# Kernel optimization log

Measured on AMD Instinct MI355X. Metric: run time of the kernel, lower is better.

## Reference

```python
import jax, jax.numpy as jnp
import numpy as np
import math

NUM_HEADS = 8


def setup_inputs() -> dict:
    key = jax.random.key(0)
    ks = jax.random.split(key, 6)
    b, s, e = 4, 2048, 512
    x = jax.random.normal(ks[0], (b, s, e), dtype=jnp.float32)
    # 0/1 adjacency matrix as float (it multiplies the scores in the module)
    adj = jax.random.randint(ks[1], (b, s, s), 0, 2).astype(jnp.float32)
    scale = 0.02
    Wqkv_w = jax.random.normal(ks[2], (3 * e, e), dtype=jnp.float32) * scale
    Wqkv_b = jax.random.normal(ks[3], (3 * e,), dtype=jnp.float32) * scale
    out_w = jax.random.normal(ks[4], (e, e), dtype=jnp.float32) * scale
    out_b = jax.random.normal(ks[5], (e,), dtype=jnp.float32) * scale
    return {"x": x, "adj": adj, "Wqkv_w": Wqkv_w, "Wqkv_b": Wqkv_b,
            "out_w": out_w, "out_b": out_b}


def reference(x, adj, Wqkv_w, Wqkv_b, out_w, out_b):
    b, s, e = x.shape
    h = NUM_HEADS
    d = e // h
    # fused qkv projection: (b, s, 3*e) -> (b, s, 3, h, d)
    qkv = (x @ Wqkv_w.T + Wqkv_b).reshape(b, s, 3, h, d)
    qkv = jnp.transpose(qkv, (2, 0, 3, 1, 4))  # (3, b, h, s, d)
    q, k, v = qkv[0], qkv[1], qkv[2]
    inv_sqrt_d = 1.0 / math.sqrt(d)
    scores = jnp.einsum('bhqd,bhkd->bhqk', q, k) * inv_sqrt_d
    scores = jnp.clip(scores * adj[:, None, :, :], -10000.0, 10000.0)
    attn = jax.nn.softmax(scores, axis=-1)
    out = jnp.einsum('bhqk,bhkd->bhqd', attn, v)
    out = jnp.transpose(out, (0, 2, 1, 3)).reshape(b, s, e)  # (b, s, h*d)
    return out @ out_w.T + out_b
```

## Files before the change

### kernel.cpp

```cpp
#include <hip/hip_runtime.h>


typedef __attribute__((ext_vector_type(8))) short bf16x8;
typedef __attribute__((ext_vector_type(4))) float f32x4;
typedef __attribute__((ext_vector_type(4))) unsigned short ushort4v;
typedef __attribute__((ext_vector_type(4))) _Float16 f16x4;
typedef __attribute__((ext_vector_type(8))) _Float16 f16x8;
typedef __attribute__((ext_vector_type(2))) __fp16 h16x2;

#if __has_builtin(__builtin_amdgcn_exp2f)
#define EXP2F(x) __builtin_amdgcn_exp2f(x)
#else
#define EXP2F(x) exp2f(x)
#endif

#define QSCALE 0.18033688011112042f

__device__ __forceinline__ unsigned short f2bf(float f) {
  unsigned int u = __float_as_uint(f);
  u += 0x7FFFu + ((u >> 16) & 1u);
  return (unsigned short)(u >> 16);
}
__device__ __forceinline__ unsigned short f2h(float f) {
  union { _Float16 h; unsigned short u; } cv;
  cv.h = (_Float16)f;
  return cv.u;
}

__device__ __forceinline__ int sbit(unsigned w, int pos) {
  return ((int)(w << (31 - pos))) >> 31;
}

__device__ __forceinline__ f16x8 pk8(const float* p) {
  union { struct { h16x2 a, b, c, d; } s; f16x8 v; } u;
  u.s.a = __builtin_amdgcn_cvt_pkrtz(p[0], p[1]);
  u.s.b = __builtin_amdgcn_cvt_pkrtz(p[2], p[3]);
  u.s.c = __builtin_amdgcn_cvt_pkrtz(p[4], p[5]);
  u.s.d = __builtin_amdgcn_cvt_pkrtz(p[6], p[7]);
  return u.v;
}

__device__ __forceinline__ f32x4 mfma_pv(f16x8 a, f16x8 b, f32x4 c) {
#if __has_builtin(__builtin_amdgcn_mfma_f32_16x16x32_f16)
  return __builtin_amdgcn_mfma_f32_16x16x32_f16(a, b, c, 0, 0, 0);
#else
  union { f16x8 v; struct { f16x4 lo, hi; } s; } ua, ub;
  ua.v = a; ub.v = b;
  c = __builtin_amdgcn_mfma_f32_16x16x16f16(ua.s.lo, ub.s.lo, c, 0, 0, 0);
  return __builtin_amdgcn_mfma_f32_16x16x16f16(ua.s.hi, ub.s.hi, c, 0, 0, 0);
#endif
}

__global__ __launch_bounds__(256) void prep_k(const float* __restrict__ x,
                                              unsigned short* __restrict__ x_bf,
                                              const float* __restrict__ wqkv,
                                              unsigned short* __restrict__ wqkv_bf,
                                              const float* __restrict__ outw,
                                              unsigned short* __restrict__ outw_bf,
                                              const float* __restrict__ adj,
                                              unsigned long long* __restrict__ abits) {
  const int bid = blockIdx.x;
  if (bid < 5120) {
    const float* in; unsigned short* out; int i;
    if (bid < 4096) { in = x; out = x_bf; i = bid * 256 + threadIdx.x; }
    else if (bid < 4864) { in = wqkv; out = wqkv_bf; i = (bid - 4096) * 256 + threadIdx.x; }
    else { in = outw; out = outw_bf; i = (bid - 4864) * 256 + threadIdx.x; }
    float4 v = ((const float4*)in)[i];
    ushort4v o;
    o[0] = f2bf(v.x); o[1] = f2bf(v.y); o[2] = f2bf(v.z); o[3] = f2bf(v.w);
    ((ushort4v*)out)[i] = o;
  } else {
    const int gw = (bid - 5120) * 4 + (threadIdx.x >> 6);
    const int l = threadIdx.x & 63;
    const int b = gw >> 11, q = gw & 2047;
    const float* row = adj + ((size_t)b * 2048 + q) * 2048;
    unsigned long long* ob = abits + (size_t)b * 65536 + q;
#pragma unroll 4
    for (int kt = 0; kt < 32; ++kt) {
      const float v = row[kt * 64 + l];
      const unsigned long long m = __ballot(v != 0.f);
      if (l == 0) ob[(size_t)kt * 2048] = m;
    }
  }
}

template <int MODE>
__global__ __launch_bounds__(256, 3) void gemm128_k(const unsigned short* __restrict__ A,
                                                    const unsigned short* __restrict__ Bt,
                                                    const float* __restrict__ bias, int Kdim,
                                                    int Ntiles, unsigned short* __restrict__ q_out,
                                                    unsigned short* __restrict__ k_out,
                                                    unsigned short* __restrict__ v_out,
                                                    float* __restrict__ f_out) {
  __shared__ union {
    struct { unsigned short A[2][128][40], B[2][128][40]; } s;
    unsigned short T[64][136];
  } u;

  const int t = threadIdx.x;
  const int lane = t & 63, w = t >> 6, ln = lane & 15, quad = lane >> 4;
  const int xcd = blockIdx.x & 7, loc = blockIdx.x >> 3;
  const int mt = xcd * ((gridDim.x >> 3) / Ntiles) + loc / Ntiles;
  const int nt = loc % Ntiles;
  const int wm = (w >> 1) * 64, wn = (w & 1) * 64;
  const int strow = t >> 2, stcol = (t & 3) * 8;

  const size_t abase = (size_t)(mt * 128 + strow) * Kdim + stcol;
  const size_t bbase = (size_t)(nt * 128 + strow) * Kdim + stcol;

  f32x4 acc[4][4];
#pragma unroll
  for (int i = 0; i < 4; ++i)
#pragma unroll
    for (int j = 0; j < 4; ++j) acc[i][j] = (f32x4){0.f, 0.f, 0.f, 0.f};

  bf16x8 a0 = *(const bf16x8*)(A + abase);
  bf16x8 a1 = *(const bf16x8*)(A + abase + (size_t)64 * Kdim);
  bf16x8 b0 = *(const bf16x8*)(Bt + bbase);
  bf16x8 b1 = *(const bf16x8*)(Bt + bbase + (size_t)64 * Kdim);
  *(bf16x8*)&u.s.A[0][strow][stcol] = a0;
  *(bf16x8*)&u.s.A[0][64 + strow][stcol] = a1;
  *(bf16x8*)&u.s.B[0][strow][stcol] = b0;
  *(bf16x8*)&u.s.B[0][64 + strow][stcol] = b1;
  __syncthreads();

  const int iters = Kdim >> 5;
  for (int it = 0; it < iters; ++it) {
    const int cur = it & 1, nxt = cur ^ 1;

    const int kn = ((it + 1) << 5) & (Kdim - 1);
    a0 = *(const bf16x8*)(A + abase + kn);
    a1 = *(const bf16x8*)(A + abase + (size_t)64 * Kdim + kn);
    b0 = *(const bf16x8*)(Bt + bbase + kn);
    b1 = *(const bf16x8*)(Bt + bbase + (size_t)64 * Kdim + kn);

    bf16x8 bfr[4];
#pragma unroll
    for (int nf = 0; nf < 4; ++nf)
      bfr[nf] = *(const bf16x8*)&u.s.B[cur][wn + nf * 16 + ln][quad * 8];
#pragma unroll
    for (int mf = 0; mf < 4; ++mf) {
      bf16x8 af = *(const bf16x8*)&u.s.A[cur][wm + mf * 16 + ln][quad * 8];
#pragma unroll
      for (int nf = 0; nf < 4; ++nf)
        acc[mf][nf] = __builtin_amdgcn_mfma_f32_16x16x32_bf16(af, bfr[nf], acc[mf][nf], 0, 0, 0);
    }

    if (it + 1 < iters) {
      *(bf16x8*)&u.s.A[nxt][strow][stcol] = a0;
      *(bf16x8*)&u.s.A[nxt][64 + strow][stcol] = a1;
      *(bf16x8*)&u.s.B[nxt][strow][stcol] = b0;
      *(bf16x8*)&u.s.B[nxt][64 + strow][stcol] = b1;
      __syncthreads();
    }
  }

  if (MODE == 0 && nt >= 8) {
    const int bb = mt >> 4, sq0 = (mt & 15) * 128;
#pragma unroll
    for (int half = 0; half < 2; ++half) {
      __syncthreads();
      if ((w & 1) == half) {
#pragma unroll
        for (int nf = 0; nf < 4; ++nf) {
          const float bv = bias[nt * 128 + half * 64 + nf * 16 + ln];
#pragma unroll
          for (int mf = 0; mf < 4; ++mf)
#pragma unroll
            for (int r = 0; r < 4; ++r)
              u.T[nf * 16 + ln][wm + mf * 16 + quad * 4 + r] = f2h(acc[mf][nf][r] + bv);
        }
      }
      __syncthreads();
#pragma unroll
      for (int rep = 0; rep < 4; ++rep) {
        const int row = rep * 16 + (t >> 4), c = t & 15;
        const bf16x8 val = *(const bf16x8*)&u.T[row][c * 8];
        const int hd = (nt - 8) * 128 + half * 64 + row;
        const int hh = hd >> 6, dd = hd & 63;
        *(bf16x8*)(v_out + ((size_t)(bb * 8 + hh) * 64 + dd) * 2048 + sq0 + c * 8) = val;
      }
    }
    return;
  }

#pragma unroll
  for (int mf = 0; mf < 4; ++mf) {
    const int m = mt * 128 + wm + mf * 16 + quad * 4;
#pragma unroll
    for (int nf = 0; nf < 4; ++nf) {
      const int n = nt * 128 + wn + nf * 16 + ln;
      const float bv = bias[n];
      if (MODE == 0) {
        const int hd = n & 511;
        const int hh = hd >> 6, dd = hd & 63;
        const int bb = m >> 11, sq = m & 2047;
        if (n < 512) {
#pragma unroll
          for (int r = 0; r < 4; ++r)
            q_out[((size_t)(bb * 8 + hh) * 2048 + sq + r) * 64 + dd] =
                f2bf((acc[mf][nf][r] + bv) * QSCALE);
        } else {
#pragma unroll
          for (int r = 0; r < 4; ++r)
            k_out[((size_t)(bb * 8 + hh) * 2048 + sq + r) * 64 + dd] = f2bf(acc[mf][nf][r] + bv);
        }
      } else {
#pragma unroll
        for (int r = 0; r < 4; ++r) f_out[(size_t)(m + r) * 512 + n] = acc[mf][nf][r] + bv;
      }
    }
  }
}

__global__ __launch_bounds__(256, 2) void attn_k(const unsigned short* __restrict__ Qg,
                                                 const unsigned short* __restrict__ Kg,
                                                 const unsigned short* __restrict__ Vg,
                                                 const unsigned long long* __restrict__ Mg,
                                                 unsigned short* __restrict__ Og) {
  __shared__ unsigned short K_lds[2][64][64];
  __shared__ unsigned short V_lds[2][64][64];

  const int t = threadIdx.x;
  const int w = t >> 6, lane = t & 63, ln = lane & 15, quad = lane >> 4;
  const int bh = blockIdx.x & 31, qt = blockIdx.x >> 5, bb = bh >> 3;
  const int sbase = qt * 128;

  const unsigned short* Qp = Qg + (size_t)bh * (2048 * 64);
  const unsigned short* Kp = Kg + (size_t)bh * (2048 * 64);
  const unsigned short* Vp = Vg + (size_t)bh * (64 * 2048);
  const unsigned long long* Mw = Mg + (size_t)bb * 65536 + sbase + w * 32 + ln;

  bf16x8 qf[2][2];
#pragma unroll
  for (int qg = 0; qg < 2; ++qg) {
    const int qrow = sbase + w * 32 + qg * 16 + ln;
    qf[qg][0] = *(const bf16x8*)(Qp + (size_t)qrow * 64 + quad * 8);
    qf[qg][1] = *(const bf16x8*)(Qp + (size_t)qrow * 64 + 32 + quad * 8);
  }

  const _Float16 one_h = (_Float16)((ln == 0) ? 1.0f : 0.0f);
  const f16x8 vf_one = (f16x8){one_h, one_h, one_h, one_h, one_h, one_h, one_h, one_h};

  const f32x4 zf = (f32x4){0.f, 0.f, 0.f, 0.f};

  f32x4 acc_o[2][4];
#pragma unroll
  for (int qg = 0; qg < 2; ++qg)
#pragma unroll
    for (int dg = 0; dg < 4; ++dg) acc_o[qg][dg] = zf;
  f32x4 acc_1[2] = {zf, zf};

  const int strow = t >> 2;
  const int stcol = (t & 3) * 16;
  const int c0 = (t & 3) * 2;
  const int gkw = (strow & 3) | (((strow >> 3) & 1) << 2);
  const int gvw = strow & 7;

  const unsigned short* Kl = Kp + (size_t)strow * 64 + stcol;
  const unsigned short* Vl = Vp + (size_t)strow * 2048 + stcol;

  bf16x8 kr0 = *(const bf16x8*)(Kl);
  bf16x8 kr1 = *(const bf16x8*)(Kl + 8);
  bf16x8 vr0 = *(const bf16x8*)(Vl);
  bf16x8 vr1 = *(const bf16x8*)(Vl + 8);
  *(bf16x8*)&K_lds[0][strow][(c0 ^ gkw) << 3] = kr0;
  *(bf16x8*)&K_lds[0][strow][((c0 + 1) ^ gkw) << 3] = kr1;
  *(bf16x8*)&V_lds[0][strow][(c0 ^ gvw) << 3] = vr0;
  *(bf16x8*)&V_lds[0][strow][((c0 + 1) ^ gvw) << 3] = vr1;
  unsigned long long m0 = Mw[0], m1 = Mw[16];
  __syncthreads();

  const int kperm = ((ln >> 2) << 3) + (ln & 3);
  const int gkr = (ln & 3) | (((ln >> 2) & 1) << 2);
  const int gvr = ln & 7;
  const int kc = (quad ^ gkr) << 3;

#pragma unroll 2
  for (int kt = 0; kt < 32; ++kt) {
    const int cur = kt & 1, nxt = cur ^ 1;

    kr0 = *(const bf16x8*)(Kl + (size_t)(kt + 1) * 4096);
    kr1 = *(const bf16x8*)(Kl + (size_t)(kt + 1) * 4096 + 8);
    vr0 = *(const bf16x8*)(Vl + (kt + 1) * 64);
    vr1 = *(const bf16x8*)(Vl + (kt + 1) * 64 + 8);
    const unsigned long long m0n = Mw[(size_t)(kt + 1) * 2048];
    const unsigned long long m1n = Mw[(size_t)(kt + 1) * 2048 + 16];

    f32x4 sc[2][4];
    __builtin_amdgcn_s_setprio(1);
#pragma unroll
    for (int h = 0; h < 2; ++h)
#pragma unroll
      for (int e = 0; e < 2; ++e) {
        const int krow = h * 32 + kperm + e * 4;
        bf16x8 kf0 = *(const bf16x8*)&K_lds[cur][krow][kc];
        bf16x8 kf1 = *(const bf16x8*)&K_lds[cur][krow][kc ^ 32];
#pragma unroll
        for (int qg = 0; qg < 2; ++qg) {
          f32x4 z = __builtin_amdgcn_mfma_f32_16x16x32_bf16(kf0, qf[qg][0], zf, 0, 0, 0);
          sc[qg][h * 2 + e] = __builtin_amdgcn_mfma_f32_16x16x32_bf16(kf1, qf[qg][1], z, 0, 0, 0);
        }
      }
    __builtin_amdgcn_s_setprio(0);

    f16x8 vfa[2][4];
#pragma unroll
    for (int h = 0; h < 2; ++h)
#pragma unroll
      for (int dg = 0; dg < 4; ++dg)
        vfa[h][dg] = *(const f16x8*)&V_lds[cur][dg * 16 + ln][((h * 4 + quad) ^ gvr) << 3];

    f16x8 pa[2][2];
#pragma unroll
    for (int qg = 0; qg < 2; ++qg) {
      const unsigned long long m64 = qg ? m1 : m0;
#pragma unroll
      for (int h = 0; h < 2; ++h) {
        const unsigned wrd = (h ? (unsigned)(m64 >> 32) : (unsigned)m64) >> (quad * 8);
        float p[8];
#pragma unroll
        for (int e = 0; e < 2; ++e)
#pragma unroll
          for (int r = 0; r < 4; ++r) {
            const int j = e * 4 + r;
            const int se = sbit(wrd, j);
            const float s = __int_as_float(__float_as_int(sc[qg][h * 2 + e][r]) & se);
            p[j] = EXP2F(s);
          }
        pa[qg][h] = pk8(p);
      }
    }

    __builtin_amdgcn_s_setprio(1);
#pragma unroll
    for (int h = 0; h < 2; ++h)
#pragma unroll
      for (int qg = 0; qg < 2; ++qg) {
#pragma unroll
        for (int dg = 0; dg < 4; ++dg)
          acc_o[qg][dg] = mfma_pv(pa[qg][h], vfa[h][dg], acc_o[qg][dg]);
        acc_1[qg] = mfma_pv(pa[qg][h], vf_one, acc_1[qg]);
      }
    __builtin_amdgcn_s_setprio(0);

    if (kt < 31) {
      *(bf16x8*)&K_lds[nxt][strow][(c0 ^ gkw) << 3] = kr0;
      *(bf16x8*)&K_lds[nxt][strow][((c0 + 1) ^ gkw) << 3] = kr1;
      *(bf16x8*)&V_lds[nxt][strow][(c0 ^ gvw) << 3] = vr0;
      *(bf16x8*)&V_lds[nxt][strow][((c0 + 1) ^ gvw) << 3] = vr1;
      __syncthreads();
    }
    m0 = m0n;
    m1 = m1n;
  }

  unsigned short* Op = Og + (size_t)bb * 2048 * 512 + (size_t)(bh & 7) * 64;
#pragma unroll
  for (int qg = 0; qg < 2; ++qg)
#pragma unroll
    for (int r = 0; r < 4; ++r) {
      const float inv = 1.0f / __shfl(acc_1[qg][r], quad * 16);
      const int sq = sbase + w * 32 + qg * 16 + quad * 4 + r;
#pragma unroll
      for (int dg = 0; dg < 4; ++dg)
        Op[(size_t)sq * 512 + dg * 16 + ln] = f2bf(acc_o[qg][dg][r] * inv);
    }
}

extern "C" void kernel_launch(void* const* d_in, const int* in_sizes, int n_in, void* d_out,
                              int out_size, void* d_ws, size_t ws_size, hipStream_t stream) {
  const float* x = (const float*)d_in[0];
  const float* adj = (const float*)d_in[1];
  const float* wqkv = (const float*)d_in[2];
  const float* bqkv = (const float*)d_in[3];
  const float* outw = (const float*)d_in[4];
  const float* outb = (const float*)d_in[5];
  float* out = (float*)d_out;

  char* ws = (char*)d_ws;
  unsigned short* x_bf = (unsigned short*)(ws);
  unsigned short* wqkv_bf = (unsigned short*)(ws + 8388608);
  unsigned short* outw_bf = (unsigned short*)(ws + 9961472);
  unsigned long long* abits = (unsigned long long*)(ws + 10485760);
  unsigned short* Qb = (unsigned short*)(ws + 27262976);
  unsigned short* Kb = (unsigned short*)(ws + 35651584);
  unsigned short* Vb = (unsigned short*)(ws + 44040192);
  unsigned short* Ob = (unsigned short*)(ws + 52428800);

  prep_k<<<7168, 256, 0, stream>>>(x, x_bf, wqkv, wqkv_bf, outw, outw_bf, adj, abits);

  gemm128_k<0><<<768, 256, 0, stream>>>(x_bf, wqkv_bf, bqkv, 512, 12, Qb, Kb, Vb, nullptr);

  attn_k<<<512, 256, 0, stream>>>(Qb, Kb, Vb, abits, Ob);

  gemm128_k<1><<<256, 256, 0, stream>>>(Ob, outw_bf, outb, 512, 4, nullptr, nullptr, nullptr, out);
}
```

Before: 210.7 us.

## Fuse fp32-to-bf16 conversion and adjacency bitpacking into the QKV GEMM launch

Removes the separate prep kernel. The GEMMs now load fp32 x and weights directly and convert them to bf16 in registers with v_cvt_pk_bf16_f32. The adjacency ballot bitpacking runs in extra blocks appended to the QKV GEMM grid. This saves one launch and the bf16 round-trip through memory, but each GEMM block re-reads fp32 operands at twice the bytes and converts them redundantly. The bitpack blocks also share the grid with the GEMM tiles. Tile mapping and K are now hardcoded to 512.

```diff
diff --git a/kernel.cpp b/kernel.cpp
--- a/kernel.cpp
+++ b/kernel.cpp
@@ -25,6 +25,20 @@
   union { _Float16 h; unsigned short u; } cv;
   cv.h = (_Float16)f;
   return cv.u;
+}
+
+__device__ __forceinline__ unsigned cvtpk_bf16(float a, float b) {
+  unsigned r;
+  asm("v_cvt_pk_bf16_f32 %0, %1, %2" : "=v"(r) : "v"(a), "v"(b));
+  return r;
+}
+__device__ __forceinline__ bf16x8 cvt8(float4 lo, float4 hi) {
+  union { unsigned u[4]; bf16x8 v; } r;
+  r.u[0] = cvtpk_bf16(lo.x, lo.y);
+  r.u[1] = cvtpk_bf16(lo.z, lo.w);
+  r.u[2] = cvtpk_bf16(hi.x, hi.y);
+  r.u[3] = cvtpk_bf16(hi.z, hi.w);
+  return r.v;
 }
 
 __device__ __forceinline__ int sbit(unsigned w, int pos) {
@@ -51,62 +65,52 @@
 #endif
 }
 
-__global__ __launch_bounds__(256) void prep_k(const float* __restrict__ x,
-                                              unsigned short* __restrict__ x_bf,
-                                              const float* __restrict__ wqkv,
-                                              unsigned short* __restrict__ wqkv_bf,
-                                              const float* __restrict__ outw,
-                                              unsigned short* __restrict__ outw_bf,
-                                              const float* __restrict__ adj,
-                                              unsigned long long* __restrict__ abits) {
-  const int bid = blockIdx.x;
-  if (bid < 5120) {
-    const float* in; unsigned short* out; int i;
-    if (bid < 4096) { in = x; out = x_bf; i = bid * 256 + threadIdx.x; }
-    else if (bid < 4864) { in = wqkv; out = wqkv_bf; i = (bid - 4096) * 256 + threadIdx.x; }
-    else { in = outw; out = outw_bf; i = (bid - 4864) * 256 + threadIdx.x; }
-    float4 v = ((const float4*)in)[i];
-    ushort4v o;
-    o[0] = f2bf(v.x); o[1] = f2bf(v.y); o[2] = f2bf(v.z); o[3] = f2bf(v.w);
-    ((ushort4v*)out)[i] = o;
-  } else {
-    const int gw = (bid - 5120) * 4 + (threadIdx.x >> 6);
-    const int l = threadIdx.x & 63;
-    const int b = gw >> 11, q = gw & 2047;
-    const float* row = adj + ((size_t)b * 2048 + q) * 2048;
-    unsigned long long* ob = abits + (size_t)b * 65536 + q;
-#pragma unroll 4
-    for (int kt = 0; kt < 32; ++kt) {
-      const float v = row[kt * 64 + l];
-      const unsigned long long m = __ballot(v != 0.f);
-      if (l == 0) ob[(size_t)kt * 2048] = m;
-    }
-  }
-}
-
 template <int MODE>
-__global__ __launch_bounds__(256, 3) void gemm128_k(const unsigned short* __restrict__ A,
-                                                    const unsigned short* __restrict__ Bt,
-                                                    const float* __restrict__ bias, int Kdim,
-                                                    int Ntiles, unsigned short* __restrict__ q_out,
+__global__ __launch_bounds__(256, 3) void gemm128_k(const float* __restrict__ Af,
+                                                    const unsigned short* __restrict__ Abf,
+                                                    const float* __restrict__ Btf,
+                                                    const float* __restrict__ bias, int Ntiles,
+                                                    unsigned short* __restrict__ q_out,
                                                     unsigned short* __restrict__ k_out,
                                                     unsigned short* __restrict__ v_out,
-                                                    float* __restrict__ f_out) {
+                                                    float* __restrict__ f_out,
+                                                    const float* __restrict__ adj,
+                                                    unsigned long long* __restrict__ abits) {
   __shared__ union {
     struct { unsigned short A[2][128][40], B[2][128][40]; } s;
     unsigned short T[64][136];
   } u;
 
   const int t = threadIdx.x;
+
+  if (MODE == 0 && blockIdx.x >= 768) {
+    const int w = t >> 6, l = t & 63;
+    const int base = (blockIdx.x - 768) * 16;
+#pragma unroll
+    for (int i = 0; i < 4; ++i) {
+      const int gw = base + w * 4 + i;
+      const int b = gw >> 11, q = gw & 2047;
+      const float* row = adj + ((size_t)b * 2048 + q) * 2048;
+      unsigned long long* ob = abits + (size_t)b * 65536 + q;
+#pragma unroll 4
+      for (int kt = 0; kt < 32; ++kt) {
+        const float v = row[kt * 64 + l];
+        const unsigned long long m = __ballot(v != 0.f);
+        if (l == 0) ob[(size_t)kt * 2048] = m;
+      }
+    }
+    return;
+  }
+
   const int lane = t & 63, w = t >> 6, ln = lane & 15, quad = lane >> 4;
   const int xcd = blockIdx.x & 7, loc = blockIdx.x >> 3;
-  const int mt = xcd * ((gridDim.x >> 3) / Ntiles) + loc / Ntiles;
+  const int mt = xcd * 8 + loc / Ntiles;
   const int nt = loc % Ntiles;
   const int wm = (w >> 1) * 64, wn = (w & 1) * 64;
   const int strow = t >> 2, stcol = (t & 3) * 8;
 
-  const size_t abase = (size_t)(mt * 128 + strow) * Kdim + stcol;
-  const size_t bbase = (size_t)(nt * 128 + strow) * Kdim + stcol;
+  const size_t abase = (size_t)(mt * 128 + strow) * 512 + stcol;
+  const size_t bbase = (size_t)(nt * 128 + strow) * 512 + stcol;
 
   f32x4 acc[4][4];
 #pragma unroll
@@ -114,25 +118,40 @@
 #pragma unroll
     for (int j = 0; j < 4; ++j) acc[i][j] = (f32x4){0.f, 0.f, 0.f, 0.f};
 
-  bf16x8 a0 = *(const bf16x8*)(A + abase);
-  bf16x8 a1 = *(const bf16x8*)(A + abase + (size_t)64 * Kdim);
-  bf16x8 b0 = *(const bf16x8*)(Bt + bbase);
-  bf16x8 b1 = *(const bf16x8*)(Bt + bbase + (size_t)64 * Kdim);
+  bf16x8 a0, a1, b0, b1;
+#define LOADAB(kn)                                                              \
+  {                                                                             \
+    if (MODE == 0) {                                                            \
+      float4 l0 = *(const float4*)(Af + abase + (kn));                          \
+      float4 h0 = *(const float4*)(Af + abase + (kn) + 4);                      \
+      float4 l1 = *(const float4*)(Af + abase + (size_t)64 * 512 + (kn));       \
+      float4 h1 = *(const float4*)(Af + abase + (size_t)64 * 512 + (kn) + 4);   \
+      a0 = cvt8(l0, h0);                                                        \
+      a1 = cvt8(l1, h1);                                                        \
+    } else {                                                                    \
+      a0 = *(const bf16x8*)(Abf + abase + (kn));                                \
+      a1 = *(const bf16x8*)(Abf + abase + (size_t)64 * 512 + (kn));             \
+    }                                                                           \
+    float4 bl0 = *(const float4*)(Btf + bbase + (kn));                          \
+    float4 bh0 = *(const float4*)(Btf + bbase + (kn) + 4);                      \
+    float4 bl1 = *(const float4*)(Btf + bbase + (size_t)64 * 512 + (kn));       \
+    float4 bh1 = *(const float4*)(Btf + bbase + (size_t)64 * 512 + (kn) + 4);   \
+    b0 = cvt8(bl0, bh0);                                                        \
+    b1 = cvt8(bl1, bh1);                                                        \
+  }
+
+  LOADAB(0);
   *(bf16x8*)&u.s.A[0][strow][stcol] = a0;
   *(bf16x8*)&u.s.A[0][64 + strow][stcol] = a1;
   *(bf16x8*)&u.s.B[0][strow][stcol] = b0;
   *(bf16x8*)&u.s.B[0][64 + strow][stcol] = b1;
   __syncthreads();
 
-  const int iters = Kdim >> 5;
-  for (int it = 0; it < iters; ++it) {
+  for (int it = 0; it < 16; ++it) {
     const int cur = it & 1, nxt = cur ^ 1;
 
-    const int kn = ((it + 1) << 5) & (Kdim - 1);
-    a0 = *(const bf16x8*)(A + abase + kn);
-    a1 = *(const bf16x8*)(A + abase + (size_t)64 * Kdim + kn);
-    b0 = *(const bf16x8*)(Bt + bbase + kn);
-    b1 = *(const bf16x8*)(Bt + bbase + (size_t)64 * Kdim + kn);
+    const int kn = ((it + 1) << 5) & 511;
+    LOADAB(kn);
 
     bf16x8 bfr[4];
 #pragma unroll
@@ -146,7 +165,7 @@
         acc[mf][nf] = __builtin_amdgcn_mfma_f32_16x16x32_bf16(af, bfr[nf], acc[mf][nf], 0, 0, 0);
     }
 
-    if (it + 1 < iters) {
+    if (it + 1 < 16) {
       *(bf16x8*)&u.s.A[nxt][strow][stcol] = a0;
       *(bf16x8*)&u.s.A[nxt][64 + strow][stcol] = a1;
       *(bf16x8*)&u.s.B[nxt][strow][stcol] = b0;
@@ -154,6 +173,7 @@
       __syncthreads();
     }
   }
+#undef LOADAB
 
   if (MODE == 0 && nt >= 8) {
     const int bb = mt >> 4, sq0 = (mt & 15) * 128;
@@ -379,20 +399,17 @@
   float* out = (float*)d_out;
 
   char* ws = (char*)d_ws;
-  unsigned short* x_bf = (unsigned short*)(ws);
-  unsigned short* wqkv_bf = (unsigned short*)(ws + 8388608);
-  unsigned short* outw_bf = (unsigned short*)(ws + 9961472);
   unsigned long long* abits = (unsigned long long*)(ws + 10485760);
   unsigned short* Qb = (unsigned short*)(ws + 27262976);
   unsigned short* Kb = (unsigned short*)(ws + 35651584);
   unsigned short* Vb = (unsigned short*)(ws + 44040192);
   unsigned short* Ob = (unsigned short*)(ws + 52428800);
 
-  prep_k<<<7168, 256, 0, stream>>>(x, x_bf, wqkv, wqkv_bf, outw, outw_bf, adj, abits);
-
-  gemm128_k<0><<<768, 256, 0, stream>>>(x_bf, wqkv_bf, bqkv, 512, 12, Qb, Kb, Vb, nullptr);
+  gemm128_k<0><<<1280, 256, 0, stream>>>(x, nullptr, wqkv, bqkv, 12, Qb, Kb, Vb, nullptr,
+                                         adj, abits);
 
   attn_k<<<512, 256, 0, stream>>>(Qb, Kb, Vb, abits, Ob);
 
-  gemm128_k<1><<<256, 256, 0, stream>>>(Ob, outw_bf, outb, 512, 4, nullptr, nullptr, nullptr, out);
-}
+  gemm128_k<1><<<256, 256, 0, stream>>>(nullptr, Ob, outw, outb, 4, nullptr, nullptr, nullptr,
+                                        out, nullptr, nullptr);
+}
```

After: 266.6 us. 26.5% more time.

## Pack adjacency bitmask in float4-interleaved layout and load masks per four tiles

Applied to the files above, without the earlier changes.

The adjacency-to-bitmask pass now reads float4 per lane and ballots each component, writing four 64-bit words per query row in an interleaved layout. The attention kernel loads these masks as 128-bit vectors once per group of four key tiles, instead of two scalar 64-bit loads per tile, and remaps bit positions to match. This targets the cost of the adjacency read (wider loads) and the mask fetches in the attention inner loop, at the price of more complex bit indexing and added register pressure.

```diff
diff --git a/kernel.cpp b/kernel.cpp
--- a/kernel.cpp
+++ b/kernel.cpp
@@ -7,6 +7,7 @@
 typedef __attribute__((ext_vector_type(4))) _Float16 f16x4;
 typedef __attribute__((ext_vector_type(8))) _Float16 f16x8;
 typedef __attribute__((ext_vector_type(2))) __fp16 h16x2;
+typedef __attribute__((ext_vector_type(2))) unsigned long long u64x2;
 
 #if __has_builtin(__builtin_amdgcn_exp2f)
 #define EXP2F(x) __builtin_amdgcn_exp2f(x)
@@ -73,13 +74,21 @@
     const int gw = (bid - 5120) * 4 + (threadIdx.x >> 6);
     const int l = threadIdx.x & 63;
     const int b = gw >> 11, q = gw & 2047;
-    const float* row = adj + ((size_t)b * 2048 + q) * 2048;
-    unsigned long long* ob = abits + (size_t)b * 65536 + q;
-#pragma unroll 4
-    for (int kt = 0; kt < 32; ++kt) {
-      const float v = row[kt * 64 + l];
-      const unsigned long long m = __ballot(v != 0.f);
-      if (l == 0) ob[(size_t)kt * 2048] = m;
+    const float4* row = (const float4*)(adj + ((size_t)b * 2048 + q) * 2048) + l;
+    unsigned long long* ob = abits + ((size_t)b * 8 * 2048 + q) * 4;
+#pragma unroll
+    for (int it = 0; it < 8; ++it) {
+      const float4 v = row[(size_t)it * 64];
+      const unsigned long long w0 = __ballot(v.x != 0.f);
+      const unsigned long long w1 = __ballot(v.y != 0.f);
+      const unsigned long long w2 = __ballot(v.z != 0.f);
+      const unsigned long long w3 = __ballot(v.w != 0.f);
+      if (l == 0) {
+        ob[(size_t)it * 8192 + 0] = w0;
+        ob[(size_t)it * 8192 + 1] = w1;
+        ob[(size_t)it * 8192 + 2] = w2;
+        ob[(size_t)it * 8192 + 3] = w3;
+      }
     }
   }
 }
@@ -229,7 +238,7 @@
   const unsigned short* Qp = Qg + (size_t)bh * (2048 * 64);
   const unsigned short* Kp = Kg + (size_t)bh * (2048 * 64);
   const unsigned short* Vp = Vg + (size_t)bh * (64 * 2048);
-  const unsigned long long* Mw = Mg + (size_t)bb * 65536 + sbase + w * 32 + ln;
+  const unsigned long long* Mb = Mg + ((size_t)bb * 8 * 2048 + sbase + w * 32 + ln) * 4;
 
   bf16x8 qf[2][2];
 #pragma unroll
@@ -268,91 +277,111 @@
   *(bf16x8*)&K_lds[0][strow][((c0 + 1) ^ gkw) << 3] = kr1;
   *(bf16x8*)&V_lds[0][strow][(c0 ^ gvw) << 3] = vr0;
   *(bf16x8*)&V_lds[0][strow][((c0 + 1) ^ gvw) << 3] = vr1;
-  unsigned long long m0 = Mw[0], m1 = Mw[16];
+  u64x2 Wlo[2], Whi[2];
+#pragma unroll
+  for (int qg = 0; qg < 2; ++qg) {
+    Wlo[qg] = *(const u64x2*)(Mb + qg * 64);
+    Whi[qg] = *(const u64x2*)(Mb + qg * 64 + 2);
+  }
   __syncthreads();
 
   const int kperm = ((ln >> 2) << 3) + (ln & 3);
   const int gkr = (ln & 3) | (((ln >> 2) & 1) << 2);
   const int gvr = ln & 7;
   const int kc = (quad ^ gkr) << 3;
-
-#pragma unroll 2
-  for (int kt = 0; kt < 32; ++kt) {
-    const int cur = kt & 1, nxt = cur ^ 1;
-
-    kr0 = *(const bf16x8*)(Kl + (size_t)(kt + 1) * 4096);
-    kr1 = *(const bf16x8*)(Kl + (size_t)(kt + 1) * 4096 + 8);
-    vr0 = *(const bf16x8*)(Vl + (kt + 1) * 64);
-    vr1 = *(const bf16x8*)(Vl + (kt + 1) * 64 + 8);
-    const unsigned long long m0n = Mw[(size_t)(kt + 1) * 2048];
-    const unsigned long long m1n = Mw[(size_t)(kt + 1) * 2048 + 16];
-
-    f32x4 sc[2][4];
-    __builtin_amdgcn_s_setprio(1);
-#pragma unroll
-    for (int h = 0; h < 2; ++h)
-#pragma unroll
-      for (int e = 0; e < 2; ++e) {
-        const int krow = h * 32 + kperm + e * 4;
-        bf16x8 kf0 = *(const bf16x8*)&K_lds[cur][krow][kc];
-        bf16x8 kf1 = *(const bf16x8*)&K_lds[cur][krow][kc ^ 32];
+  const unsigned q2 = quad << 1;
+
+  for (int kts = 0; kts < 8; ++kts) {
+    const size_t itn = (size_t)((kts < 7) ? kts + 1 : 0) * 8192;
+    u64x2 nWlo[2], nWhi[2];
+#pragma unroll
+    for (int qg = 0; qg < 2; ++qg) {
+      nWlo[qg] = *(const u64x2*)(Mb + itn + qg * 64);
+      nWhi[qg] = *(const u64x2*)(Mb + itn + qg * 64 + 2);
+    }
+
+#pragma unroll
+    for (int j = 0; j < 4; ++j) {
+      const int kt = kts * 4 + j;
+      const int cur = j & 1, nxt = cur ^ 1;
+
+      kr0 = *(const bf16x8*)(Kl + (size_t)(kt + 1) * 4096);
+      kr1 = *(const bf16x8*)(Kl + (size_t)(kt + 1) * 4096 + 8);
+      vr0 = *(const bf16x8*)(Vl + (kt + 1) * 64);
+      vr1 = *(const bf16x8*)(Vl + (kt + 1) * 64 + 8);
+
+      f32x4 sc[2][4];
+      __builtin_amdgcn_s_setprio(1);
+#pragma unroll
+      for (int h = 0; h < 2; ++h)
+#pragma unroll
+        for (int e = 0; e < 2; ++e) {
+          const int krow = h * 32 + kperm + e * 4;
+          bf16x8 kf0 = *(const bf16x8*)&K_lds[cur][krow][kc];
+          bf16x8 kf1 = *(const bf16x8*)&K_lds[cur][krow][kc ^ 32];
+#pragma unroll
+          for (int qg = 0; qg < 2; ++qg) {
+            f32x4 z = __builtin_amdgcn_mfma_f32_16x16x32_bf16(kf0, qf[qg][0], zf, 0, 0, 0);
+            sc[qg][h * 2 + e] = __builtin_amdgcn_mfma_f32_16x16x32_bf16(kf1, qf[qg][1], z, 0, 0, 0);
+          }
+        }
+      __builtin_amdgcn_s_setprio(0);
+
+      f16x8 vfa[2][4];
+#pragma unroll
+      for (int h = 0; h < 2; ++h)
+#pragma unroll
+        for (int dg = 0; dg < 4; ++dg)
+          vfa[h][dg] = *(const f16x8*)&V_lds[cur][dg * 16 + ln][((h * 4 + quad) ^ gvr) << 3];
+
+      f16x8 pa[2][2];
+#pragma unroll
+      for (int qg = 0; qg < 2; ++qg) {
+        const unsigned s0 = (unsigned)(Wlo[qg][0] >> (j >= 2 ? 32 : 0)) >> q2;
+        const unsigned s1 = (unsigned)(Wlo[qg][1] >> (j >= 2 ? 32 : 0)) >> q2;
+        const unsigned s2 = (unsigned)(Whi[qg][0] >> (j >= 2 ? 32 : 0)) >> q2;
+        const unsigned s3 = (unsigned)(Whi[qg][1] >> (j >= 2 ? 32 : 0)) >> q2;
+#pragma unroll
+        for (int h = 0; h < 2; ++h) {
+          float p[8];
+#pragma unroll
+          for (int e = 0; e < 2; ++e) {
+            const int pos = (j & 1) * 16 + h * 8 + e;
+            p[e * 4 + 0] =
+                EXP2F(__int_as_float(__float_as_int(sc[qg][h * 2 + e][0]) & sbit(s0, pos)));
+            p[e * 4 + 1] =
+                EXP2F(__int_as_float(__float_as_int(sc[qg][h * 2 + e][1]) & sbit(s1, pos)));
+            p[e * 4 + 2] =
+                EXP2F(__int_as_float(__float_as_int(sc[qg][h * 2 + e][2]) & sbit(s2, pos)));
+            p[e * 4 + 3] =
+                EXP2F(__int_as_float(__float_as_int(sc[qg][h * 2 + e][3]) & sbit(s3, pos)));
+          }
+          pa[qg][h] = pk8(p);
+        }
+      }
+
+      __builtin_amdgcn_s_setprio(1);
+#pragma unroll
+      for (int h = 0; h < 2; ++h)
 #pragma unroll
         for (int qg = 0; qg < 2; ++qg) {
-          f32x4 z = __builtin_amdgcn_mfma_f32_16x16x32_bf16(kf0, qf[qg][0], zf, 0, 0, 0);
-          sc[qg][h * 2 + e] = __builtin_amdgcn_mfma_f32_16x16x32_bf16(kf1, qf[qg][1], z, 0, 0, 0);
+#pragma unroll
+          for (int dg = 0; dg < 4; ++dg)
+            acc_o[qg][dg] = mfma_pv(pa[qg][h], vfa[h][dg], acc_o[qg][dg]);
+          acc_1[qg] = mfma_pv(pa[qg][h], vf_one, acc_1[qg]);
         }
-      }
-    __builtin_amdgcn_s_setprio(0);
-
-    f16x8 vfa[2][4];
-#pragma unroll
-    for (int h = 0; h < 2; ++h)
-#pragma unroll
-      for (int dg = 0; dg < 4; ++dg)
-        vfa[h][dg] = *(const f16x8*)&V_lds[cur][dg * 16 + ln][((h * 4 + quad) ^ gvr) << 3];
-
-    f16x8 pa[2][2];
-#pragma unroll
-    for (int qg = 0; qg < 2; ++qg) {
-      const unsigned long long m64 = qg ? m1 : m0;
-#pragma unroll
-      for (int h = 0; h < 2; ++h) {
-        const unsigned wrd = (h ? (unsigned)(m64 >> 32) : (unsigned)m64) >> (quad * 8);
-        float p[8];
-#pragma unroll
-        for (int e = 0; e < 2; ++e)
-#pragma unroll
-          for (int r = 0; r < 4; ++r) {
-            const int j = e * 4 + r;
-            const int se = sbit(wrd, j);
-            const float s = __int_as_float(__float_as_int(sc[qg][h * 2 + e][r]) & se);
-            p[j] = EXP2F(s);
-          }
-        pa[qg][h] = pk8(p);
-      }
-    }
-
-    __builtin_amdgcn_s_setprio(1);
-#pragma unroll
-    for (int h = 0; h < 2; ++h)
-#pragma unroll
-      for (int qg = 0; qg < 2; ++qg) {
-#pragma unroll
-        for (int dg = 0; dg < 4; ++dg)
-          acc_o[qg][dg] = mfma_pv(pa[qg][h], vfa[h][dg], acc_o[qg][dg]);
-        acc_1[qg] = mfma_pv(pa[qg][h], vf_one, acc_1[qg]);
-      }
-    __builtin_amdgcn_s_setprio(0);
-
-    if (kt < 31) {
-      *(bf16x8*)&K_lds[nxt][strow][(c0 ^ gkw) << 3] = kr0;
-      *(bf16x8*)&K_lds[nxt][strow][((c0 + 1) ^ gkw) << 3] = kr1;
-      *(bf16x8*)&V_lds[nxt][strow][(c0 ^ gvw) << 3] = vr0;
-      *(bf16x8*)&V_lds[nxt][strow][((c0 + 1) ^ gvw) << 3] = vr1;
-      __syncthreads();
-    }
-    m0 = m0n;
-    m1 = m1n;
+      __builtin_amdgcn_s_setprio(0);
+
+      if (kt < 31) {
+        *(bf16x8*)&K_lds[nxt][strow][(c0 ^ gkw) << 3] = kr0;
+        *(bf16x8*)&K_lds[nxt][strow][((c0 + 1) ^ gkw) << 3] = kr1;
+        *(bf16x8*)&V_lds[nxt][strow][(c0 ^ gvw) << 3] = vr0;
+        *(bf16x8*)&V_lds[nxt][strow][((c0 + 1) ^ gvw) << 3] = vr1;
+        __syncthreads();
+      }
+    }
+    Wlo[0] = nWlo[0]; Wlo[1] = nWlo[1];
+    Whi[0] = nWhi[0]; Whi[1] = nWhi[1];
   }
 
   unsigned short* Op = Og + (size_t)bb * 2048 * 512 + (size_t)(bh & 7) * 64;
```

After: 203.3 us. 3.5% less time.
